# Kernel tuning notes

Measured on AMD Instinct MI355X. Metric: run time of the kernel, lower is better.

The kernel has to match this reference:

```python
import jax, jax.numpy as jnp
import numpy as np

N_NODES = 100000
N_EDGES = 1600000
IN_C = 128
HID = 128
OUT_C = 10
NUM_GRAPHS = 512


def _glorot(key, shape):
    lim = float(np.sqrt(6.0 / (shape[0] + shape[1])))
    return jax.random.uniform(key, shape, jnp.float32, -lim, lim)


def setup_inputs() -> dict:
    key = jax.random.key(0)
    ks = jax.random.split(key, 12)
    x = jax.random.normal(ks[0], (N_NODES, IN_C), jnp.float32)
    edge_index = jax.random.randint(ks[1], (2, N_EDGES), 0, N_NODES, jnp.int64)
    batch = jnp.sort(jax.random.randint(ks[2], (N_NODES,), 0, NUM_GRAPHS, jnp.int64))
    return {
        'x': x, 'edge_index': edge_index, 'batch': batch,
        'Wc0': _glorot(ks[3], (IN_C, HID)), 'bc0': jnp.zeros((HID,), jnp.float32),
        'Wc1': _glorot(ks[4], (HID, HID)), 'bc1': jnp.zeros((HID,), jnp.float32),
        'Wc2': _glorot(ks[5], (HID, HID)), 'bc2': jnp.zeros((HID,), jnp.float32),
        'W1': _glorot(ks[6], (HID, HID)), 'b1': jnp.zeros((HID,), jnp.float32),
        'W2': _glorot(ks[7], (HID, OUT_C)), 'b2': jnp.zeros((OUT_C,), jnp.float32),
    }


def _gcn_conv(x, src, dst, W, b, n):
    # PyG GCNConv: add self-loops, symmetric norm D^-1/2 (A+I) D^-1/2, then XW + b.
    # deg includes the self-loop (+1); messages flow src -> dst.
    deg = jax.ops.segment_sum(jnp.ones((src.shape[0],), x.dtype), dst, num_segments=n) + 1.0
    dinv = jax.lax.rsqrt(deg)  # deg >= 1 so no zeros
    h = x @ W  # [N, H]
    coef = dinv[src] * dinv[dst]  # [E]
    agg = jax.ops.segment_sum(h[src] * coef[:, None], dst, num_segments=n)
    agg = agg + h * (dinv * dinv)[:, None]  # self-loop contribution, no edge materialization
    return agg + b


def reference(x, edge_index, batch, Wc0, bc0, Wc1, bc1, Wc2, bc2, W1, b1, W2, b2):
    n = x.shape[0]
    src, dst = edge_index[0], edge_index[1]
    # eval mode: dropout is identity
    h = jax.nn.relu(_gcn_conv(x, src, dst, Wc0, bc0, n))
    h = jax.nn.relu(_gcn_conv(h, src, dst, Wc1, bc1, n))
    h = _gcn_conv(h, src, dst, Wc2, bc2, n)
    # global_mean_pool over graphs
    sums = jax.ops.segment_sum(h, batch, num_segments=NUM_GRAPHS)
    counts = jax.ops.segment_sum(jnp.ones((n,), h.dtype), batch, num_segments=NUM_GRAPHS)
    pooled = sums / jnp.maximum(counts, 1.0)[:, None]  # [G, H]
    out = jax.nn.relu(pooled @ W1 + b1)
    return out @ W2 + b2  # [G, OUT_C]
```

## Files before the change

kernel.cpp:

```cpp
#include <hip/hip_runtime.h>
#include <hip/hip_bf16.h>
#include <stdint.h>

#define HID     128
#define OUTC    10
#define NGRAPH  512
#define NGROUP  64
#define PSIZE   256
#define CAP     160

using bf16x8 = __attribute__((ext_vector_type(8))) short;
using f32x4  = __attribute__((ext_vector_type(4))) float;
using u32x4  = __attribute__((ext_vector_type(4))) uint32_t;

__device__ __forceinline__ short f2bf(float f) {
    __hip_bfloat16 h = __float2bfloat16(f);
    return *reinterpret_cast<short*>(&h);
}
__device__ __forceinline__ float bf2f(short s) {
    union { uint32_t u; float f; } x; x.u = ((uint32_t)(uint16_t)s) << 16; return x.f;
}
__device__ __forceinline__ float bflo(uint32_t v) {
    union { uint32_t u; float f; } x; x.u = v << 16; return x.f;
}
__device__ __forceinline__ float bfhi(uint32_t v) {
    union { uint32_t u; float f; } x; x.u = v & 0xffff0000u; return x.f;
}
__device__ __forceinline__ uint32_t pk2(float lo, float hi) {
    return (uint32_t)(uint16_t)f2bf(lo) | ((uint32_t)(uint16_t)f2bf(hi) << 16);
}

__device__ __forceinline__ int detect_f64(const int* __restrict__ ei) {
    int lane = threadIdx.x & 63;
    int v = ei[2 * lane + 1];
    unsigned long long b = __ballot(v == 0);
    return (b == ~0ULL) ? 1 : 0;
}

__device__ __forceinline__ int fetch_idx(const int* __restrict__ p, long j, int f64) {
    return p[f64 ? (j << 1) : j];
}

__global__ void __launch_bounds__(256) prep_kernel(
        const int* __restrict__ ei, const int* __restrict__ batch,
        const float* __restrict__ W0, const float* __restrict__ W1,
        const float* __restrict__ W2, short* __restrict__ Wt,
        int* __restrict__ cnt, int cntN, int* __restrict__ gstart, int n) {
    __shared__ float Ws[64][129];
    int bid = blockIdx.x;
    const int tid = threadIdx.x;

    if (bid < 3) {
        const float* W = (bid == 0) ? W0 : (bid == 1) ? W1 : W2;
        short* hi = Wt + (size_t)bid * 2 * HID * HID;
        short* lo = hi + HID * HID;
        for (int half = 0; half < 2; ++half) {
            const int kbase = half * 64;
#pragma unroll
            for (int it = 0; it < 8; ++it) {
                int idx = (tid + it * 256) * 4;
                int k = idx >> 7, c = idx & 127;
                float4 v = *(const float4*)(W + (size_t)(kbase + k) * HID + c);
                Ws[k][c] = v.x; Ws[k][c + 1] = v.y; Ws[k][c + 2] = v.z; Ws[k][c + 3] = v.w;
            }
            __syncthreads();
            const int k2 = tid & 63;
            const int cb = tid >> 6;
#pragma unroll
            for (int it = 0; it < 32; ++it) {
                int c = cb + it * 4;
                float w = Ws[k2][c];
                short h = f2bf(w);
                hi[(size_t)c * HID + kbase + k2] = h;
                lo[(size_t)c * HID + kbase + k2] = f2bf(w - bf2f(h));
            }
            __syncthreads();
        }
        return;
    }
    bid -= 3;
    const int nzb = (cntN + 255) / 256;
    if (bid < nzb) {
        int i = bid * 256 + tid;
        if (i < cntN) cnt[i] = 0;
        return;
    }
    bid -= nzb;
    const int f = detect_f64(ei);
    int i = bid * 256 + tid;
    if (i >= n) return;
    int b  = fetch_idx(batch, i, f);
    int bp = (i == 0) ? -1 : fetch_idx(batch, i - 1, f);
    for (int g = bp + 1; g <= b; ++g) gstart[g] = i;
    if (i == n - 1) {
        for (int g = b + 1; g <= NGRAPH; ++g) gstart[g] = n;
    }
}

__global__ void __launch_bounds__(256) bin_scatter_kernel(
        const int* __restrict__ ei, int* __restrict__ cnt,
        uint32_t* __restrict__ binned, long E, int NBIN, int NBINP) {
    const int group = blockIdx.x & (NGROUP - 1);
    const int f = detect_f64(ei);
    const long stride = (long)gridDim.x * blockDim.x;
    for (long e = (long)blockIdx.x * blockDim.x + threadIdx.x; e < E; e += stride) {
        int s = fetch_idx(ei, e, f);
        int d = fetch_idx(ei, E + e, f);
        int b = d >> 8;
        int pos = atomicAdd(&cnt[group * NBINP + b], 1);
        if (pos < CAP)
            binned[((size_t)group * NBIN + b) * CAP + pos] =
                (uint32_t)s | ((uint32_t)(d & (PSIZE - 1)) << 20);
    }
}

__global__ void __launch_bounds__(1024) binscan_kernel(
        const int* __restrict__ cnt, int* __restrict__ bofs, int NBIN, int NBINP) {
    __shared__ int wsum[16];
    const int tid  = threadIdx.x;
    const int lane = tid & 63;
    const int wid  = tid >> 6;
    int v = 0;
    if (tid < NBIN) {
        for (int g = 0; g < NGROUP; ++g) v += cnt[g * NBINP + tid];
    }
    int inc = v;
#pragma unroll
    for (int d = 1; d < 64; d <<= 1) {
        int t = __shfl_up(inc, d, 64);
        if (lane >= d) inc += t;
    }
    if (lane == 63) wsum[wid] = inc;
    __syncthreads();
    if (wid == 0) {
        int ws = (lane < 16) ? wsum[lane] : 0;
        int winc = ws;
#pragma unroll
        for (int d = 1; d < 16; d <<= 1) {
            int t = __shfl_up(winc, d, 64);
            if (lane >= d) winc += t;
        }
        if (lane < 16) wsum[lane] = winc - ws;
    }
    __syncthreads();
    int excl = wsum[wid] + (inc - v);
    if (tid <= NBIN) bofs[tid] = excl;
}

__global__ void __launch_bounds__(512) bin_build_kernel(
        const uint32_t* __restrict__ binned, const int* __restrict__ cnt,
        const int* __restrict__ bofs, int* __restrict__ ofs,
        float* __restrict__ dinv, int* __restrict__ col,
        int n, int NBIN, int NBINP, long E) {
    __shared__ int lcnt[PSIZE];
    __shared__ int lofs[PSIZE];
    __shared__ int lrank[PSIZE];
    __shared__ int wtot[4];
    const int b    = blockIdx.x;
    const int v0   = b * PSIZE;
    const int nn   = min(PSIZE, n - v0);
    const int tid  = threadIdx.x;
    const int wv   = tid >> 6;
    const int lane = tid & 63;
    if (tid < PSIZE) { lcnt[tid] = 0; lrank[tid] = 0; }
    __syncthreads();
    for (int sg = wv; sg < NGROUP; sg += 8) {
        const int c = min(cnt[sg * NBINP + b], CAP);
        const uint32_t* __restrict__ src = binned + ((size_t)sg * NBIN + b) * CAP;
        for (int i = lane; i < c; i += 64)
            atomicAdd(&lcnt[src[i] >> 20], 1);
    }
    __syncthreads();
    if (tid < PSIZE) {
        int v = lcnt[tid];
        int inc = v;
#pragma unroll
        for (int d = 1; d < 64; d <<= 1) {
            int t = __shfl_up(inc, d, 64);
            if (lane >= d) inc += t;
        }
        if (lane == 63) wtot[wv] = inc;
        lofs[tid] = inc - v;
    }
    __syncthreads();
    if (tid < PSIZE) {
        int add = 0;
#pragma unroll
        for (int k = 0; k < 4; ++k) if (k < wv) add += wtot[k];
        lofs[tid] += add;
    }
    __syncthreads();
    const int base = bofs[b];
    for (int sg = wv; sg < NGROUP; sg += 8) {
        const int c = min(cnt[sg * NBINP + b], CAP);
        const uint32_t* __restrict__ src = binned + ((size_t)sg * NBIN + b) * CAP;
        for (int i = lane; i < c; i += 64) {
            uint32_t v = src[i];
            int dl = (int)(v >> 20);
            int rk = atomicAdd(&lrank[dl], 1);
            col[base + lofs[dl] + rk] = (int)(v & 0xFFFFFu);
        }
    }
    if (tid < nn) {
        ofs[v0 + tid]  = base + lofs[tid];
        dinv[v0 + tid] = rsqrtf((float)lcnt[tid] + 1.0f);
    }
    if (tid == 0 && v0 + nn == n) ofs[n] = (int)E;
}

template<bool AFP32>
__global__ void __launch_bounds__(256) gemm_hs_kernel(
        const void* __restrict__ Ap, const short* __restrict__ Wt,
        const float* __restrict__ dinv, short* __restrict__ hs, int n) {
    __shared__ __attribute__((aligned(16))) short As[128 * 128];
    const short* __restrict__ Bh = Wt;
    const short* __restrict__ Bl = Wt + HID * HID;
    const int tid = threadIdx.x;
    const int w  = tid >> 6;
    const int l  = tid & 63;
    const int lr = l & 15;
    const int kq = l >> 4;
    const int r0 = blockIdx.x * 128;

    const float* Af = (const float*)Ap;
    const short* Ab = (const short*)Ap;

#pragma unroll
    for (int it = 0; it < 8; ++it) {
        int ci  = tid + it * 256;
        int row = ci >> 4, c = ci & 15;
        int rg  = r0 + row; if (rg >= n) rg = n - 1;
        bf16x8 tv;
        if (AFP32) {
            const float* ap = Af + (size_t)rg * HID + c * 8;
            float4 f0 = *(const float4*)ap;
            float4 f1 = *(const float4*)(ap + 4);
            tv[0] = f2bf(f0.x); tv[1] = f2bf(f0.y); tv[2] = f2bf(f0.z); tv[3] = f2bf(f0.w);
            tv[4] = f2bf(f1.x); tv[5] = f2bf(f1.y); tv[6] = f2bf(f1.z); tv[7] = f2bf(f1.w);
        } else {
            tv = *(const bf16x8*)(Ab + (size_t)rg * HID + c * 8);
        }
        *(bf16x8*)(As + row * 128 + ((c ^ (row & 15)) << 3)) = tv;
    }
    __syncthreads();

    f32x4 acc[8][2] = {};
    const int col0 = w * 32 + lr;
    const int col1 = w * 32 + 16 + lr;

#pragma unroll
    for (int ks = 0; ks < 4; ++ks) {
        const int k0 = ks * 32 + kq * 8;
        bf16x8 a[8];
#pragma unroll
        for (int rf = 0; rf < 8; ++rf) {
            int row = rf * 16 + lr;
            a[rf] = *(const bf16x8*)(As + row * 128 + (((ks * 4 + kq) ^ lr) << 3));
        }
        bf16x8 bh0 = *(const bf16x8*)(Bh + (size_t)col0 * HID + k0);
        bf16x8 bh1 = *(const bf16x8*)(Bh + (size_t)col1 * HID + k0);
        bf16x8 bl0 = *(const bf16x8*)(Bl + (size_t)col0 * HID + k0);
        bf16x8 bl1 = *(const bf16x8*)(Bl + (size_t)col1 * HID + k0);
#pragma unroll
        for (int rf = 0; rf < 8; ++rf) {
            acc[rf][0] = __builtin_amdgcn_mfma_f32_16x16x32_bf16(a[rf], bh0, acc[rf][0], 0, 0, 0);
            acc[rf][1] = __builtin_amdgcn_mfma_f32_16x16x32_bf16(a[rf], bh1, acc[rf][1], 0, 0, 0);
            acc[rf][0] = __builtin_amdgcn_mfma_f32_16x16x32_bf16(a[rf], bl0, acc[rf][0], 0, 0, 0);
            acc[rf][1] = __builtin_amdgcn_mfma_f32_16x16x32_bf16(a[rf], bl1, acc[rf][1], 0, 0, 0);
        }
    }
#pragma unroll
    for (int rf = 0; rf < 8; ++rf) {
#pragma unroll
        for (int rg = 0; rg < 4; ++rg) {
            int row = r0 + rf * 16 + kq * 4 + rg;
            if (row < n) {
                float dn = dinv[row];
                hs[(size_t)row * HID + col0] = f2bf(acc[rf][0][rg] * dn);
                hs[(size_t)row * HID + col1] = f2bf(acc[rf][1][rg] * dn);
            }
        }
    }
}

__device__ __forceinline__ void acc_add(float* acc, u32x4 v) {
    acc[0] += bflo(v.x); acc[1] += bfhi(v.x);
    acc[2] += bflo(v.y); acc[3] += bfhi(v.y);
    acc[4] += bflo(v.z); acc[5] += bfhi(v.z);
    acc[6] += bflo(v.w); acc[7] += bfhi(v.w);
}

__global__ void __launch_bounds__(256) agg_kernel(
        const short* __restrict__ hs, const float* __restrict__ dinv,
        const int* __restrict__ ofs, const int* __restrict__ col,
        const float* __restrict__ bias, short* __restrict__ out,
        int n, int do_relu) {
    int node = blockIdx.x * 4 + (threadIdx.x >> 6);
    if (node >= n) return;
    const int lane = threadIdx.x & 63;
    const int g    = lane >> 4;
    const int sub  = lane & 15;
    const u32x4* __restrict__ rows = (const u32x4*)hs;

    float acc[8] = {0.f, 0.f, 0.f, 0.f, 0.f, 0.f, 0.f, 0.f};
    if (g == 0) {
        u32x4 sv = rows[(size_t)node * 16 + sub];
        acc_add(acc, sv);
    }
    const int e0 = ofs[node], e1 = ofs[node + 1];
    int e = e0;
    for (; e + 16 <= e1; e += 16) {
        int c0 = col[e + g];
        int c1 = col[e + 4 + g];
        int c2 = col[e + 8 + g];
        int c3 = col[e + 12 + g];
        u32x4 v0 = rows[(size_t)c0 * 16 + sub];
        u32x4 v1 = rows[(size_t)c1 * 16 + sub];
        u32x4 v2 = rows[(size_t)c2 * 16 + sub];
        u32x4 v3 = rows[(size_t)c3 * 16 + sub];
        acc_add(acc, v0); acc_add(acc, v1); acc_add(acc, v2); acc_add(acc, v3);
    }
    for (; e + 4 <= e1; e += 4) {
        int c0 = col[e + g];
        u32x4 v0 = rows[(size_t)c0 * 16 + sub];
        acc_add(acc, v0);
    }
    if (e + g < e1) {
        int c0 = col[e + g];
        u32x4 v0 = rows[(size_t)c0 * 16 + sub];
        acc_add(acc, v0);
    }
#pragma unroll
    for (int i = 0; i < 8; ++i) {
        acc[i] += __shfl_xor(acc[i], 16, 64);
        acc[i] += __shfl_xor(acc[i], 32, 64);
    }
    if (g == 0) {
        const float dn = dinv[node];
        float4 b0 = *(const float4*)(bias + 8 * sub);
        float4 b1 = *(const float4*)(bias + 8 * sub + 4);
        float o0 = fmaf(acc[0], dn, b0.x);
        float o1 = fmaf(acc[1], dn, b0.y);
        float o2 = fmaf(acc[2], dn, b0.z);
        float o3 = fmaf(acc[3], dn, b0.w);
        float o4 = fmaf(acc[4], dn, b1.x);
        float o5 = fmaf(acc[5], dn, b1.y);
        float o6 = fmaf(acc[6], dn, b1.z);
        float o7 = fmaf(acc[7], dn, b1.w);
        if (do_relu) {
            o0 = fmaxf(o0, 0.f); o1 = fmaxf(o1, 0.f);
            o2 = fmaxf(o2, 0.f); o3 = fmaxf(o3, 0.f);
            o4 = fmaxf(o4, 0.f); o5 = fmaxf(o5, 0.f);
            o6 = fmaxf(o6, 0.f); o7 = fmaxf(o7, 0.f);
        }
        u32x4 pk;
        pk.x = pk2(o0, o1); pk.y = pk2(o2, o3);
        pk.z = pk2(o4, o5); pk.w = pk2(o6, o7);
        ((u32x4*)out)[(size_t)node * 16 + sub] = pk;
    }
}

__global__ void __launch_bounds__(128) pool_mlp_kernel(
        const short* __restrict__ h, const int* __restrict__ gstart,
        const float* __restrict__ W1, const float* __restrict__ b1,
        const float* __restrict__ W2, const float* __restrict__ b2,
        float* __restrict__ out) {
    __shared__ float p[HID];
    __shared__ float hid[HID];
    int g = blockIdx.x, c = threadIdx.x;
    int s = gstart[g], e = gstart[g + 1];
    float acc = 0.f;
    int i = s;
    for (; i + 4 <= e; i += 4) {
        acc += bf2f(h[(size_t)i * HID + c]) + bf2f(h[(size_t)(i + 1) * HID + c])
             + bf2f(h[(size_t)(i + 2) * HID + c]) + bf2f(h[(size_t)(i + 3) * HID + c]);
    }
    for (; i < e; ++i) acc += bf2f(h[(size_t)i * HID + c]);
    p[c] = acc / fmaxf((float)(e - s), 1.f);
    __syncthreads();
    float a = b1[c];
#pragma unroll 8
    for (int k = 0; k < HID; ++k) a = fmaf(p[k], W1[k * HID + c], a);
    hid[c] = fmaxf(a, 0.f);
    __syncthreads();
    if (c < OUTC) {
        float o = b2[c];
#pragma unroll 8
        for (int k = 0; k < HID; ++k) o = fmaf(hid[k], W2[k * OUTC + c], o);
        out[g * OUTC + c] = o;
    }
}

extern "C" void kernel_launch(void* const* d_in, const int* in_sizes, int n_in,
                              void* d_out, int out_size, void* d_ws, size_t ws_size,
                              hipStream_t stream) {
    const float* x   = (const float*)d_in[0];
    const int*   ei  = (const int*)d_in[1];
    const int*   bat = (const int*)d_in[2];
    const float* Wc0 = (const float*)d_in[3];
    const float* bc0 = (const float*)d_in[4];
    const float* Wc1 = (const float*)d_in[5];
    const float* bc1 = (const float*)d_in[6];
    const float* Wc2 = (const float*)d_in[7];
    const float* bc2 = (const float*)d_in[8];
    const float* W1  = (const float*)d_in[9];
    const float* b1  = (const float*)d_in[10];
    const float* W2  = (const float*)d_in[11];
    const float* b2  = (const float*)d_in[12];
    float* out = (float*)d_out;

    const int  n = in_sizes[0] / HID;
    const long E = in_sizes[1] / 2;
    const int  NBIN  = (n + PSIZE - 1) / PSIZE;
    const int  NBINP = (NBIN + 15) & ~15;
    const int  cntN  = NGROUP * NBINP;

    char* w = (char*)d_ws;
    size_t off = 0;
    auto carve = [&](size_t bytes) {
        void* p = w + off;
        off += (bytes + 255) & ~(size_t)255;
        return p;
    };
    int*   cnt     = (int*)carve((size_t)cntN * 4);
    int*   bofs    = (int*)carve((size_t)(NBIN + 1) * 4);
    int*   ofs     = (int*)carve((size_t)(n + 1) * 4);
    float* dinv    = (float*)carve((size_t)n * 4);
    int*   gstart  = (int*)carve((NGRAPH + 1) * 4);
    int*   col     = (int*)carve((size_t)E * 4);
    short* Wt      = (short*)carve((size_t)3 * 2 * HID * HID * 2);
    short* hs      = (short*)carve((size_t)n * HID * 2);
    short* h       = (short*)carve((size_t)n * HID * 2);
    uint32_t* binned = (uint32_t*)h;

    const int nzb = (cntN + 255) / 256;
    const int nbb = (n + 255) / 256;
    prep_kernel<<<3 + nzb + nbb, 256, 0, stream>>>(ei, bat, Wc0, Wc1, Wc2,
                                                   Wt, cnt, cntN, gstart, n);

    bin_scatter_kernel<<<2048, 256, 0, stream>>>(ei, cnt, binned, E, NBIN, NBINP);
    binscan_kernel<<<1, 1024, 0, stream>>>(cnt, bofs, NBIN, NBINP);
    bin_build_kernel<<<NBIN, 512, 0, stream>>>(binned, cnt, bofs, ofs, dinv, col,
                                               n, NBIN, NBINP, E);

    const int gb = (n + 127) / 128;
    const int ab = (n + 3) / 4;
    const size_t WSTRIDE = (size_t)2 * HID * HID;
    gemm_hs_kernel<true><<<gb, 256, 0, stream>>>(x, Wt, dinv, hs, n);
    agg_kernel<<<ab, 256, 0, stream>>>(hs, dinv, ofs, col, bc0, h, n, 1);
    gemm_hs_kernel<false><<<gb, 256, 0, stream>>>(h, Wt + WSTRIDE, dinv, hs, n);
    agg_kernel<<<ab, 256, 0, stream>>>(hs, dinv, ofs, col, bc1, h, n, 1);
    gemm_hs_kernel<false><<<gb, 256, 0, stream>>>(h, Wt + 2 * WSTRIDE, dinv, hs, n);
    agg_kernel<<<ab, 256, 0, stream>>>(hs, dinv, ofs, col, bc2, h, n, 0);

    pool_mlp_kernel<<<NGRAPH, 128, 0, stream>>>(h, gstart, W1, b1, W2, b2, out);
}
```

Measured before the change: 372.1 us.

## Privatize edge binning in shared memory per block, dropping global atomic counters

Edge binning by destination block now runs on 256 blocks. Each block takes a contiguous chunk of edges, bins it into a large shared-memory buffer using LDS atomics, then writes the bins and their counts to global memory. The global atomicAdd counters go away, and so does the separate zeroing of those counters. Bin storage gets its own workspace buffer in bin-major layout instead of aliasing the h buffer, and binscan now reduces per-bin counts with wave shuffles. The cost is a big LDS footprint (about 100KB per block), which limits occupancy to one block per CU. The per-(group,bin) capacity also shrinks to 64, which risks dropping edges if a chunk has unusually many edges into one bin.

```diff
diff --git a/kernel.cpp b/kernel.cpp
--- a/kernel.cpp
+++ b/kernel.cpp
@@ -5,9 +5,10 @@
 #define HID     128
 #define OUTC    10
 #define NGRAPH  512
-#define NGROUP  64
+#define NGROUP  256
 #define PSIZE   256
-#define CAP     160
+#define CAP     64
+#define NBIN_MX 400
 
 using bf16x8 = __attribute__((ext_vector_type(8))) short;
 using f32x4  = __attribute__((ext_vector_type(4))) float;
@@ -45,7 +46,7 @@
         const int* __restrict__ ei, const int* __restrict__ batch,
         const float* __restrict__ W0, const float* __restrict__ W1,
         const float* __restrict__ W2, short* __restrict__ Wt,
-        int* __restrict__ cnt, int cntN, int* __restrict__ gstart, int n) {
+        int* __restrict__ gstart, int n) {
     __shared__ float Ws[64][129];
     int bid = blockIdx.x;
     const int tid = threadIdx.x;
@@ -79,13 +80,6 @@
         return;
     }
     bid -= 3;
-    const int nzb = (cntN + 255) / 256;
-    if (bid < nzb) {
-        int i = bid * 256 + tid;
-        if (i < cntN) cnt[i] = 0;
-        return;
-    }
-    bid -= nzb;
     const int f = detect_f64(ei);
     int i = bid * 256 + tid;
     if (i >= n) return;
@@ -97,33 +91,54 @@
     }
 }
 
-__global__ void __launch_bounds__(256) bin_scatter_kernel(
+__global__ void __launch_bounds__(512) bin_scatter_kernel(
         const int* __restrict__ ei, int* __restrict__ cnt,
-        uint32_t* __restrict__ binned, long E, int NBIN, int NBINP) {
-    const int group = blockIdx.x & (NGROUP - 1);
-    const int f = detect_f64(ei);
-    const long stride = (long)gridDim.x * blockDim.x;
-    for (long e = (long)blockIdx.x * blockDim.x + threadIdx.x; e < E; e += stride) {
+        uint32_t* __restrict__ binned, long E, int NBIN) {
+    __shared__ int      lcnt[NBIN_MX];
+    __shared__ uint32_t lbin[NBIN_MX * CAP];
+    const int g   = blockIdx.x;
+    const int tid = threadIdx.x;
+    const int f   = detect_f64(ei);
+    for (int b = tid; b < NBIN; b += 512) lcnt[b] = 0;
+    __syncthreads();
+    const long chunk = (E + gridDim.x - 1) / gridDim.x;
+    const long e0 = (long)g * chunk;
+    const long e1 = (e0 + chunk < E) ? e0 + chunk : E;
+    for (long e = e0 + tid; e < e1; e += 512) {
         int s = fetch_idx(ei, e, f);
         int d = fetch_idx(ei, E + e, f);
         int b = d >> 8;
-        int pos = atomicAdd(&cnt[group * NBINP + b], 1);
-        if (pos < CAP)
-            binned[((size_t)group * NBIN + b) * CAP + pos] =
-                (uint32_t)s | ((uint32_t)(d & (PSIZE - 1)) << 20);
+        int p = atomicAdd(&lcnt[b], 1);
+        if (p < CAP)
+            lbin[b * CAP + p] = (uint32_t)s | ((uint32_t)(d & (PSIZE - 1)) << 20);
+    }
+    __syncthreads();
+    const int wv = tid >> 6, lane = tid & 63;
+    for (int b = wv; b < NBIN; b += 8) {
+        int c = min(lcnt[b], CAP);
+        uint32_t* __restrict__ dst = binned + ((size_t)b * NGROUP + g) * CAP;
+        for (int i = lane; i < c; i += 64) dst[i] = lbin[b * CAP + i];
+        if (lane == 0) cnt[b * NGROUP + g] = c;
     }
 }
 
 __global__ void __launch_bounds__(1024) binscan_kernel(
-        const int* __restrict__ cnt, int* __restrict__ bofs, int NBIN, int NBINP) {
+        const int* __restrict__ cnt, int* __restrict__ bofs, int NBIN) {
+    __shared__ int stot[NBIN_MX];
     __shared__ int wsum[16];
     const int tid  = threadIdx.x;
     const int lane = tid & 63;
     const int wid  = tid >> 6;
-    int v = 0;
-    if (tid < NBIN) {
-        for (int g = 0; g < NGROUP; ++g) v += cnt[g * NBINP + tid];
-    }
+    for (int b = wid; b < NBIN; b += 16) {
+        int s = 0;
+#pragma unroll
+        for (int i = 0; i < NGROUP / 64; ++i) s += cnt[b * NGROUP + lane + i * 64];
+#pragma unroll
+        for (int d = 1; d < 64; d <<= 1) s += __shfl_xor(s, d, 64);
+        if (lane == 0) stot[b] = s;
+    }
+    __syncthreads();
+    int v = (tid < NBIN) ? stot[tid] : 0;
     int inc = v;
 #pragma unroll
     for (int d = 1; d < 64; d <<= 1) {
@@ -151,7 +166,7 @@
         const uint32_t* __restrict__ binned, const int* __restrict__ cnt,
         const int* __restrict__ bofs, int* __restrict__ ofs,
         float* __restrict__ dinv, int* __restrict__ col,
-        int n, int NBIN, int NBINP, long E) {
+        int n, int NBIN, long E) {
     __shared__ int lcnt[PSIZE];
     __shared__ int lofs[PSIZE];
     __shared__ int lrank[PSIZE];
@@ -165,8 +180,8 @@
     if (tid < PSIZE) { lcnt[tid] = 0; lrank[tid] = 0; }
     __syncthreads();
     for (int sg = wv; sg < NGROUP; sg += 8) {
-        const int c = min(cnt[sg * NBINP + b], CAP);
-        const uint32_t* __restrict__ src = binned + ((size_t)sg * NBIN + b) * CAP;
+        const int c = min(cnt[b * NGROUP + sg], CAP);
+        const uint32_t* __restrict__ src = binned + ((size_t)b * NGROUP + sg) * CAP;
         for (int i = lane; i < c; i += 64)
             atomicAdd(&lcnt[src[i] >> 20], 1);
     }
@@ -192,8 +207,8 @@
     __syncthreads();
     const int base = bofs[b];
     for (int sg = wv; sg < NGROUP; sg += 8) {
-        const int c = min(cnt[sg * NBINP + b], CAP);
-        const uint32_t* __restrict__ src = binned + ((size_t)sg * NBIN + b) * CAP;
+        const int c = min(cnt[b * NGROUP + sg], CAP);
+        const uint32_t* __restrict__ src = binned + ((size_t)b * NGROUP + sg) * CAP;
         for (int i = lane; i < c; i += 64) {
             uint32_t v = src[i];
             int dl = (int)(v >> 20);
@@ -411,9 +426,7 @@
 
     const int  n = in_sizes[0] / HID;
     const long E = in_sizes[1] / 2;
-    const int  NBIN  = (n + PSIZE - 1) / PSIZE;
-    const int  NBINP = (NBIN + 15) & ~15;
-    const int  cntN  = NGROUP * NBINP;
+    const int  NBIN = (n + PSIZE - 1) / PSIZE;
 
     char* w = (char*)d_ws;
     size_t off = 0;
@@ -422,26 +435,24 @@
         off += (bytes + 255) & ~(size_t)255;
         return p;
     };
-    int*   cnt     = (int*)carve((size_t)cntN * 4);
+    int*   cnt     = (int*)carve((size_t)NBIN * NGROUP * 4);
     int*   bofs    = (int*)carve((size_t)(NBIN + 1) * 4);
     int*   ofs     = (int*)carve((size_t)(n + 1) * 4);
     float* dinv    = (float*)carve((size_t)n * 4);
     int*   gstart  = (int*)carve((NGRAPH + 1) * 4);
     int*   col     = (int*)carve((size_t)E * 4);
     short* Wt      = (short*)carve((size_t)3 * 2 * HID * HID * 2);
+    uint32_t* binned = (uint32_t*)carve((size_t)NBIN * NGROUP * CAP * 4);
     short* hs      = (short*)carve((size_t)n * HID * 2);
     short* h       = (short*)carve((size_t)n * HID * 2);
-    uint32_t* binned = (uint32_t*)h;
-
-    const int nzb = (cntN + 255) / 256;
+
     const int nbb = (n + 255) / 256;
-    prep_kernel<<<3 + nzb + nbb, 256, 0, stream>>>(ei, bat, Wc0, Wc1, Wc2,
-                                                   Wt, cnt, cntN, gstart, n);
-
-    bin_scatter_kernel<<<2048, 256, 0, stream>>>(ei, cnt, binned, E, NBIN, NBINP);
-    binscan_kernel<<<1, 1024, 0, stream>>>(cnt, bofs, NBIN, NBINP);
+    prep_kernel<<<3 + nbb, 256, 0, stream>>>(ei, bat, Wc0, Wc1, Wc2, Wt, gstart, n);
+
+    bin_scatter_kernel<<<NGROUP, 512, 0, stream>>>(ei, cnt, binned, E, NBIN);
+    binscan_kernel<<<1, 1024, 0, stream>>>(cnt, bofs, NBIN);
     bin_build_kernel<<<NBIN, 512, 0, stream>>>(binned, cnt, bofs, ofs, dinv, col,
-                                               n, NBIN, NBINP, E);
+                                               n, NBIN, E);
 
     const int gb = (n + 127) / 128;
     const int ab = (n + 3) / 4;
```

Result: no change. 375.9 us (+1.0%).
